# Optimization experiments

Measured on AMD Instinct MI355X. Metric: run time of the kernel, lower is better.

## Reference

```python
import jax, jax.numpy as jnp
import numpy as np


def dwconv1d(u, w, b):
    # u: (B, C, L), w: (C, 1, 3) depthwise, padding=1 -> same length
    out = jax.lax.conv_general_dilated(
        u, w, window_strides=(1,), padding=[(1, 1)],
        dimension_numbers=('NCH', 'OIH', 'NCH'),
        feature_group_count=u.shape[1])
    return out + b[None, :, None]


def selective_scan(u, delta, A, Bm, Cm, D, delta_bias):
    # u, delta: (B, KD, L); A: (KD, N); Bm, Cm: (B, K, N, L); D, delta_bias: (KD,)
    Bsz, KD, L = u.shape
    K, N = Bm.shape[1], Bm.shape[2]
    Dg = KD // K
    delta = jax.nn.softplus(delta + delta_bias[None, :, None])
    Bexp = jnp.repeat(Bm, Dg, axis=1)  # (B, KD, N, L)
    Cexp = jnp.repeat(Cm, Dg, axis=1)
    dA = jnp.exp(delta[:, :, None, :] * A[None, :, :, None])        # (B, KD, N, L)
    dBu = delta[:, :, None, :] * Bexp * u[:, :, None, :]            # (B, KD, N, L)

    def step(h, inp):
        a, bu, c = inp
        h = a * h + bu
        return h, jnp.sum(h * c, axis=-1)

    a_t = jnp.moveaxis(dA, -1, 0)
    bu_t = jnp.moveaxis(dBu, -1, 0)
    c_t = jnp.moveaxis(Cexp, -1, 0)
    _, ys = jax.lax.scan(step, jnp.zeros((Bsz, KD, N), u.dtype), (a_t, bu_t, c_t))
    return jnp.moveaxis(ys, 0, -1) + D[None, :, None] * u           # (B, KD, L)


def setup_inputs():
    key = jax.random.key(0)
    ks = jax.random.split(key, 8)
    d_inner, d_state, dt_rank, K = 192, 16, 6, 1
    bincounts = np.array([4096, 3000, 3500, 2500])
    total = int(bincounts.sum())
    max_bin = int(bincounts.max())
    starts = np.concatenate([[0], np.cumsum(bincounts)[:-1]])
    # compute_padding: wrap-around padded gather indices per cloud
    padded_idx = np.concatenate([np.arange(max_bin) % bc + st for bc, st in zip(bincounts, starts)])
    # crop-back indices into the (B*max_bin) padded layout
    valid_idx = np.concatenate([i * max_bin + np.arange(bc) for i, bc in enumerate(bincounts)])
    order = np.stack([np.random.RandomState(0).permutation(total)])
    inverse = np.argsort(order, axis=1)
    x = jax.random.normal(ks[0], (d_inner, total), jnp.float32)
    x_proj_weight = jax.random.normal(ks[1], (K, dt_rank + 2 * d_state, d_inner), jnp.float32) * 0.05
    dt_projs_weight = jax.random.normal(ks[2], (K, d_inner, dt_rank), jnp.float32) * 0.1
    dt_projs_bias = jax.random.normal(ks[3], (K, d_inner), jnp.float32) * 0.1
    A_logs = jnp.log(jnp.tile(jnp.arange(1, d_state + 1, dtype=jnp.float32), (K * d_inner, 1)))
    Ds = jnp.ones((K * d_inner,), jnp.float32)
    conv_w = jax.random.normal(ks[4], (K * d_inner, 1, 3), jnp.float32) * 0.2
    conv_b = jnp.zeros((K * d_inner,), jnp.float32)
    ln_gamma = jnp.ones((d_inner,), jnp.float32)
    ln_beta = jnp.zeros((d_inner,), jnp.float32)
    return {
        'x': x, 'x_proj_weight': x_proj_weight, 'dt_projs_weight': dt_projs_weight,
        'dt_projs_bias': dt_projs_bias, 'A_logs': A_logs, 'Ds': Ds,
        'conv_w': conv_w, 'conv_b': conv_b, 'ln_gamma': ln_gamma, 'ln_beta': ln_beta,
        'order': jnp.asarray(order, jnp.int32), 'inverse': jnp.asarray(inverse, jnp.int32),
        'padded_idx': jnp.asarray(padded_idx, jnp.int32),
        'valid_idx': jnp.asarray(valid_idx, jnp.int32), 'max_bin': max_bin,
    }


def reference(x, x_proj_weight, dt_projs_weight, dt_projs_bias, A_logs, Ds,
              conv_w, conv_b, ln_gamma, ln_beta,
              order, inverse, padded_idx, valid_idx, max_bin):
    K, Dch, R = dt_projs_weight.shape
    N = A_logs.shape[1]
    BM = padded_idx.shape[0]
    Bsz = BM // max_bin
    # multi-directional gather with offset padding: x[:, order[k]][:, padded_idx]
    idx = jnp.take(order, padded_idx, axis=1)                       # (K, B*max_bin)
    xs = jnp.take(x, idx, axis=1)                                   # (Dch, K, B*max_bin)
    xs = xs.transpose(1, 0, 2).reshape(K, Dch, Bsz, max_bin).transpose(2, 0, 1, 3)  # (B,K,D,L)
    x_dbl = jnp.einsum('bkdl,kcd->bkcl', xs, x_proj_weight)         # (B,K,R+2N,L)
    dts, Bs, Cs = jnp.split(x_dbl, [R, R + N], axis=2)
    dts = jnp.einsum('bkrl,kdr->bkdl', dts, dt_projs_weight)
    u = xs.reshape(Bsz, K * Dch, max_bin)
    delta = dts.reshape(Bsz, K * Dch, max_bin)
    A = -jnp.exp(A_logs)
    u = dwconv1d(u, conv_w, conv_b)  # conv1d applied after x_dbl/dts, before scan
    ys = selective_scan(u, delta, A, Bs, Cs, Ds, dt_projs_bias.reshape(-1))  # (B, K*Dch, L)
    # crop padding per cloud and concat along points
    ys = ys.reshape(Bsz, K, Dch, max_bin).transpose(1, 2, 0, 3).reshape(K, Dch, BM)
    ys = jnp.take(ys, valid_idx, axis=2)                            # (K, Dch, total)
    # K == 1, y_proj_weight is None -> scatter back through inverse permutation
    y = jnp.take(ys[0], inverse[0], axis=1)                         # (Dch, total)
    y = y.T                                                         # (total, Dch)
    mu = jnp.mean(y, axis=-1, keepdims=True)
    var = jnp.var(y, axis=-1, keepdims=True)
    y = (y - mu) / jnp.sqrt(var + 1e-5) * ln_gamma + ln_beta        # LayerNorm(d_inner)
    return y
```

## Files before the change

kernel.cpp:

```cpp
#include <hip/hip_runtime.h>
#include <math.h>

#define DINNER 192
#define NST    16
#define RNK    6
#define LSEQ   4096
#define BSZ    4
#define TOTAL  13096
#define BMPAD  16384
#define CL     32
#define MAXC   128
#define NSTATE 3072
#define NCHAIN 12288
#define NB32   410

#define BC_OF(b)  ((b)==0?4096:(b)==1?3000:(b)==2?3500:2500)
#define QST_OF(b) ((b)==0?0:(b)==1?4096:(b)==2?7096:10596)
#define NCB_OF(b) ((b)==0?128:(b)==1?94:(b)==2?110:79)

__device__ float  g_xs[(size_t)TOTAL * DINNER];
__device__ float  g_BC[(size_t)TOTAL * 32];
__device__ float  g_dt[(size_t)TOTAL * 8];
__device__ float2 g_PQ[(size_t)BSZ * MAXC * NSTATE];
__device__ float  g_hin[(size_t)BSZ * MAXC * NSTATE];

__global__ __launch_bounds__(256) void kA(
    const float* __restrict__ x, const float* __restrict__ W,
    const int* __restrict__ inverse)
{
    const int blk = blockIdx.x;
    const int t = threadIdx.x;
    const bool isG = (blk >= NB32);
    const int P0 = (isG ? blk - NB32 : blk) * 32;
    const int npts = min(32, TOTAL - P0);

    __shared__ float sx[32 * 193];
    __shared__ float sW[38 * DINNER];
    __shared__ int   sg[32];

    if (t < 32) sg[t] = (t < npts) ? inverse[P0 + t] : 0;

    float xt[24];
    #pragma unroll
    for (int k = 0; k < 24; ++k) {
        int idx = t + k * 256;
        int j = idx & 31, d = idx >> 5;
        xt[k] = (j < npts) ? x[(size_t)d * TOTAL + P0 + j] : 0.f;
    }
    float wt[29];
    if (isG) {
        #pragma unroll
        for (int k = 0; k < 29; ++k) {
            int idx = t + k * 256;
            wt[k] = (idx < 38 * DINNER) ? W[idx] : 0.f;
        }
    }
    #pragma unroll
    for (int k = 0; k < 24; ++k) {
        int idx = t + k * 256;
        int j = idx & 31, d = idx >> 5;
        sx[j * 193 + d] = xt[k];
    }
    if (isG) {
        #pragma unroll
        for (int k = 0; k < 29; ++k) {
            int idx = t + k * 256;
            if (idx < 38 * DINNER) sW[idx] = wt[k];
        }
    }
    __syncthreads();

    if (!isG) {
        for (int idx = t; idx < npts * 48; idx += 256) {
            int j = idx / 48, q = idx - j * 48;
            const float* sp = &sx[j * 193 + q * 4];
            float4 v = {sp[0], sp[1], sp[2], sp[3]};
            *(float4*)&g_xs[(size_t)sg[j] * DINNER + q * 4] = v;
        }
    } else {
        const int j = t & 31, cw = t >> 5;
        float acc[5] = {0.f, 0.f, 0.f, 0.f, 0.f};
        for (int dt0 = 0; dt0 < DINNER; dt0 += 16) {
            float xr[16];
            #pragma unroll
            for (int q = 0; q < 16; ++q) xr[q] = sx[j * 193 + dt0 + q];
            #pragma unroll
            for (int k = 0; k < 5; ++k) {
                const int c = cw + 8 * k;
                if (c < RNK + 2 * NST) {
                    const float4* wr = (const float4*)&sW[c * DINNER + dt0];
                    float4 w0 = wr[0], w1 = wr[1], w2 = wr[2], w3 = wr[3];
                    float a = acc[k];
                    a += xr[0]*w0.x + xr[1]*w0.y + xr[2]*w0.z + xr[3]*w0.w;
                    a += xr[4]*w1.x + xr[5]*w1.y + xr[6]*w1.z + xr[7]*w1.w;
                    a += xr[8]*w2.x + xr[9]*w2.y + xr[10]*w2.z + xr[11]*w2.w;
                    a += xr[12]*w3.x + xr[13]*w3.y + xr[14]*w3.z + xr[15]*w3.w;
                    acc[k] = a;
                }
            }
        }
        if (j < npts) {
            const int g = sg[j];
            #pragma unroll
            for (int k = 0; k < 5; ++k) {
                const int c = cw + 8 * k;
                if (c < RNK)                g_dt[(size_t)g * 8 + c] = acc[k];
                else if (c < RNK + 2 * NST) g_BC[(size_t)g * 32 + (c - RNK)] = acc[k];
            }
        }
    }
}

__global__ __launch_bounds__(192) void k2_scan1(
    const float* __restrict__ A_logs, const float* __restrict__ conv_w,
    const float* __restrict__ conv_b, const float* __restrict__ dtW,
    const float* __restrict__ dtB)
{
    const int blk = blockIdx.x;
    const int b = blk >> 7;
    const int chunk = blk & (MAXC - 1);
    const int bc = BC_OF(b), qst = QST_OF(b), ncb = NCB_OF(b);
    if (chunk >= ncb) return;
    const int l0 = chunk * CL;
    const int steps = min(CL, bc - l0);
    const int t = threadIdx.x;

    __shared__ float sxr[(CL + 2) * DINNER];
    __shared__ float sB[CL * NST];
    __shared__ float sdt[CL * 8];

    float xr[CL + 2];
    #pragma unroll
    for (int k = 0; k < CL + 2; ++k) {
        int pos = l0 - 1 + k;
        bool v = (k < steps + 2) && (pos >= 0) && (pos < LSEQ);
        int pw = (pos >= bc) ? pos - bc : pos;
        xr[k] = v ? g_xs[(size_t)(qst + pw) * DINNER + t] : 0.f;
    }
    float bv[3];
    #pragma unroll
    for (int k = 0; k < 3; ++k) {
        int idx = t + k * 192;
        bv[k] = (idx < steps * NST)
              ? g_BC[(size_t)(qst + l0 + (idx >> 4)) * 32 + (idx & 15)] : 0.f;
    }
    float dv[2];
    #pragma unroll
    for (int k = 0; k < 2; ++k) {
        int idx = t + k * 192;
        dv[k] = (idx < steps * 8) ? g_dt[(size_t)(qst + l0) * 8 + idx] : 0.f;
    }
    #pragma unroll
    for (int k = 0; k < CL + 2; ++k) sxr[k * DINNER + t] = xr[k];
    #pragma unroll
    for (int k = 0; k < 3; ++k) {
        int idx = t + k * 192;
        if (idx < CL * NST) sB[idx] = bv[k];
    }
    #pragma unroll
    for (int k = 0; k < 2; ++k) {
        int idx = t + k * 192;
        if (idx < CL * 8) sdt[idx] = dv[k];
    }
    __syncthreads();

    float Av[16];
    {
        const float4* A4 = (const float4*)(A_logs + t * NST);
        #pragma unroll
        for (int q = 0; q < 4; ++q) {
            float4 v = A4[q];
            Av[q*4+0] = -__expf(v.x); Av[q*4+1] = -__expf(v.y);
            Av[q*4+2] = -__expf(v.z); Av[q*4+3] = -__expf(v.w);
        }
    }
    const float Av0 = Av[0];
    bool fast = true;
    #pragma unroll
    for (int n = 0; n < 16; ++n)
        fast = fast && (fabsf(Av[n] - (float)(n + 1) * Av0) <= 1e-4f * (float)(n + 1));

    float wdt[RNK];
    #pragma unroll
    for (int r = 0; r < RNK; ++r) wdt[r] = dtW[t * RNK + r];
    const float bdel = dtB[t];
    const float cw0 = conv_w[t*3+0], cw1 = conv_w[t*3+1], cw2 = conv_w[t*3+2];
    const float cb = conv_b[t];

    float h[16];
    #pragma unroll
    for (int n = 0; n < 16; ++n) h[n] = 0.f;
    float delsum = 0.f;
    float xm = sxr[t], xc = sxr[DINNER + t];

    for (int i = 0; i < steps; ++i) {
        float xp = sxr[(i + 2) * DINNER + t];
        float u = fmaf(cw0, xm, fmaf(cw1, xc, fmaf(cw2, xp, cb)));
        float da = bdel;
        #pragma unroll
        for (int r = 0; r < RNK; ++r) da = fmaf(wdt[r], sdt[i * 8 + r], da);
        float del = (da > 20.f) ? da : log1pf(__expf(da));
        float du = del * u;
        delsum += del;
        const float4* b4 = (const float4*)&sB[i * NST];
        float4 B0 = b4[0], B1 = b4[1], B2 = b4[2], B3 = b4[3];
        const float Bv[16] = {B0.x,B0.y,B0.z,B0.w, B1.x,B1.y,B1.z,B1.w,
                              B2.x,B2.y,B2.z,B2.w, B3.x,B3.y,B3.z,B3.w};
        if (fast) {
            float e = __expf(del * Av0);
            float a = e;
            #pragma unroll
            for (int n = 0; n < 16; ++n) { h[n] = fmaf(a, h[n], Bv[n] * du); a *= e; }
        } else {
            #pragma unroll
            for (int n = 0; n < 16; ++n) {
                float a = __expf(del * Av[n]);
                h[n] = fmaf(a, h[n], Bv[n] * du);
            }
        }
        xm = xc; xc = xp;
    }

    float4* o4 = (float4*)(g_PQ + (size_t)(b * MAXC + chunk) * NSTATE + t * 16);
    #pragma unroll
    for (int k = 0; k < 8; ++k) {
        float P0v = __expf(Av[2*k]   * delsum);
        float P1v = __expf(Av[2*k+1] * delsum);
        o4[k] = make_float4(P0v, h[2*k], P1v, h[2*k+1]);
    }
}

__global__ __launch_bounds__(128) void k3_comb()
{
    const int gid = blockIdx.x * 128 + threadIdx.x;
    const int b = gid / NSTATE;
    const int s = gid - b * NSTATE;
    const int ncb = NCB_OF(b);
    float h = 0.f;
    for (int c0 = 0; c0 < MAXC; c0 += 16) {
        if (c0 >= ncb) break;
        float2 v[16];
        #pragma unroll
        for (int k = 0; k < 16; ++k) {
            int c = c0 + k;
            v[k] = (c < ncb) ? g_PQ[(size_t)(b * MAXC + c) * NSTATE + s]
                             : make_float2(1.f, 0.f);
        }
        #pragma unroll
        for (int k = 0; k < 16; ++k) {
            int c = c0 + k;
            if (c < ncb) g_hin[(size_t)(b * MAXC + c) * NSTATE + s] = h;
            h = fmaf(v[k].x, h, v[k].y);
        }
    }
}

__global__ __launch_bounds__(192) void k4_scan2(
    const float* __restrict__ A_logs, const float* __restrict__ conv_w,
    const float* __restrict__ conv_b, const float* __restrict__ dtW,
    const float* __restrict__ dtB, const float* __restrict__ Ds,
    const int* __restrict__ order, const float* __restrict__ gamma,
    const float* __restrict__ beta, float* __restrict__ out)
{
    const int blk = blockIdx.x;
    const int b = blk >> 7;
    const int chunk = blk & (MAXC - 1);
    const int bc = BC_OF(b), qst = QST_OF(b), ncb = NCB_OF(b);
    if (chunk >= ncb) return;
    const int l0 = chunk * CL;
    const int steps = min(CL, bc - l0);
    const int t = threadIdx.x;

    __shared__ float sxr[(CL + 2) * DINNER];
    __shared__ float sBC[CL * 32];
    __shared__ float sdt[CL * 8];
    __shared__ float sy[CL * DINNER];

    float xr[CL + 2];
    #pragma unroll
    for (int k = 0; k < CL + 2; ++k) {
        int pos = l0 - 1 + k;
        bool v = (k < steps + 2) && (pos >= 0) && (pos < LSEQ);
        int pw = (pos >= bc) ? pos - bc : pos;
        xr[k] = v ? g_xs[(size_t)(qst + pw) * DINNER + t] : 0.f;
    }
    float bcv[6];
    #pragma unroll
    for (int k = 0; k < 6; ++k) {
        int idx = t + k * 192;
        bcv[k] = (idx < steps * 32) ? g_BC[(size_t)(qst + l0) * 32 + idx] : 0.f;
    }
    float dv[2];
    #pragma unroll
    for (int k = 0; k < 2; ++k) {
        int idx = t + k * 192;
        dv[k] = (idx < steps * 8) ? g_dt[(size_t)(qst + l0) * 8 + idx] : 0.f;
    }
    float h[16];
    {
        const float4* h4 = (const float4*)(g_hin + (size_t)(b * MAXC + chunk) * NSTATE + t * 16);
        #pragma unroll
        for (int q = 0; q < 4; ++q) *(float4*)&h[q * 4] = h4[q];
    }
    #pragma unroll
    for (int k = 0; k < CL + 2; ++k) sxr[k * DINNER + t] = xr[k];
    #pragma unroll
    for (int k = 0; k < 6; ++k) {
        int idx = t + k * 192;
        if (idx < CL * 32) sBC[idx] = bcv[k];
    }
    #pragma unroll
    for (int k = 0; k < 2; ++k) {
        int idx = t + k * 192;
        if (idx < CL * 8) sdt[idx] = dv[k];
    }
    __syncthreads();

    float Av[16];
    {
        const float4* A4 = (const float4*)(A_logs + t * NST);
        #pragma unroll
        for (int q = 0; q < 4; ++q) {
            float4 v = A4[q];
            Av[q*4+0] = -__expf(v.x); Av[q*4+1] = -__expf(v.y);
            Av[q*4+2] = -__expf(v.z); Av[q*4+3] = -__expf(v.w);
        }
    }
    const float Av0 = Av[0];
    bool fast = true;
    #pragma unroll
    for (int n = 0; n < 16; ++n)
        fast = fast && (fabsf(Av[n] - (float)(n + 1) * Av0) <= 1e-4f * (float)(n + 1));

    float wdt[RNK];
    #pragma unroll
    for (int r = 0; r < RNK; ++r) wdt[r] = dtW[t * RNK + r];
    const float bdel = dtB[t];
    const float cw0 = conv_w[t*3+0], cw1 = conv_w[t*3+1], cw2 = conv_w[t*3+2];
    const float cb = conv_b[t];
    const float Dd = Ds[t];

    float xm = sxr[t], xc = sxr[DINNER + t];

    for (int i = 0; i < steps; ++i) {
        float xp = sxr[(i + 2) * DINNER + t];
        float u = fmaf(cw0, xm, fmaf(cw1, xc, fmaf(cw2, xp, cb)));
        float da = bdel;
        #pragma unroll
        for (int r = 0; r < RNK; ++r) da = fmaf(wdt[r], sdt[i * 8 + r], da);
        float del = (da > 20.f) ? da : log1pf(__expf(da));
        float du = del * u;
        const float4* b4 = (const float4*)&sBC[i * 32];
        float4 B0 = b4[0], B1 = b4[1], B2 = b4[2], B3 = b4[3];
        float4 C0 = b4[4], C1 = b4[5], C2 = b4[6], C3 = b4[7];
        const float Bv[16] = {B0.x,B0.y,B0.z,B0.w, B1.x,B1.y,B1.z,B1.w,
                              B2.x,B2.y,B2.z,B2.w, B3.x,B3.y,B3.z,B3.w};
        const float Cv[16] = {C0.x,C0.y,C0.z,C0.w, C1.x,C1.y,C1.z,C1.w,
                              C2.x,C2.y,C2.z,C2.w, C3.x,C3.y,C3.z,C3.w};
        float y = Dd * u;
        if (fast) {
            float e = __expf(del * Av0);
            float a = e;
            #pragma unroll
            for (int n = 0; n < 16; ++n) {
                h[n] = fmaf(a, h[n], Bv[n] * du);
                y = fmaf(h[n], Cv[n], y);
                a *= e;
            }
        } else {
            #pragma unroll
            for (int n = 0; n < 16; ++n) {
                float a = __expf(del * Av[n]);
                h[n] = fmaf(a, h[n], Bv[n] * du);
                y = fmaf(h[n], Cv[n], y);
            }
        }
        sy[i * DINNER + t] = y;
        xm = xc; xc = xp;
    }
    __syncthreads();

    const int wv = t >> 6;
    const int lane = t & 63;
    for (int i = wv; i < steps; i += 3) {
        const float v0 = sy[i * DINNER + lane];
        const float v1 = sy[i * DINNER + 64 + lane];
        const float v2 = sy[i * DINNER + 128 + lane];
        float s  = v0 + v1 + v2;
        float s2 = v0 * v0 + v1 * v1 + v2 * v2;
        #pragma unroll
        for (int off = 1; off < 64; off <<= 1) {
            s  += __shfl_xor(s,  off);
            s2 += __shfl_xor(s2, off);
        }
        const float mu   = s / (float)DINNER;
        const float var  = s2 / (float)DINNER - mu * mu;
        const float rstd = rsqrtf(var + 1e-5f);
        const int p = order[qst + l0 + i];
        float* orow = out + (size_t)p * DINNER;
        orow[lane]       = (v0 - mu) * rstd * gamma[lane]       + beta[lane];
        orow[lane + 64]  = (v1 - mu) * rstd * gamma[lane + 64]  + beta[lane + 64];
        orow[lane + 128] = (v2 - mu) * rstd * gamma[lane + 128] + beta[lane + 128];
    }
}

extern "C" void kernel_launch(void* const* d_in, const int* in_sizes, int n_in,
                              void* d_out, int out_size, void* d_ws, size_t ws_size,
                              hipStream_t stream) {
    const float* x       = (const float*)d_in[0];
    const float* W       = (const float*)d_in[1];
    const float* dtW     = (const float*)d_in[2];
    const float* dtB     = (const float*)d_in[3];
    const float* A_logs  = (const float*)d_in[4];
    const float* Ds      = (const float*)d_in[5];
    const float* conv_w  = (const float*)d_in[6];
    const float* conv_b  = (const float*)d_in[7];
    const float* gamma   = (const float*)d_in[8];
    const float* beta    = (const float*)d_in[9];
    const int*   order   = (const int*)d_in[10];
    const int*   inverse = (const int*)d_in[11];
    float* outp = (float*)d_out;

    if (in_sizes[0] != TOTAL * DINNER || in_sizes[12] != BMPAD) return;

    kA<<<2 * NB32, 256, 0, stream>>>(x, W, inverse);
    k2_scan1<<<BSZ * MAXC, 192, 0, stream>>>(A_logs, conv_w, conv_b, dtW, dtB);
    k3_comb<<<NCHAIN / 128, 128, 0, stream>>>();
    k4_scan2<<<BSZ * MAXC, 192, 0, stream>>>(A_logs, conv_w, conv_b, dtW, dtB,
                                             Ds, order, gamma, beta, outp);
}
```

Baseline: 178.7 us.

## Merge kA gather/projection blocks, keep x window in registers, use power tree

```diff
diff --git a/kernel.cpp b/kernel.cpp
--- a/kernel.cpp
+++ b/kernel.cpp
@@ -24,15 +24,21 @@
 __device__ float2 g_PQ[(size_t)BSZ * MAXC * NSTATE];
 __device__ float  g_hin[(size_t)BSZ * MAXC * NSTATE];
 
+#define POWER_TREE(e, a)                                                   \
+    { float e1 = (e);                                                      \
+      float e2 = e1*e1, e4 = e2*e2, e8 = e4*e4;                            \
+      a[0]=e1;      a[1]=e2;      a[2]=e2*e1;   a[3]=e4;                   \
+      a[4]=e4*e1;   a[5]=e4*e2;   a[6]=e4*a[2]; a[7]=e8;                   \
+      a[8]=e8*e1;   a[9]=e8*e2;   a[10]=e8*a[2];a[11]=e8*e4;               \
+      a[12]=e8*a[4];a[13]=e8*a[5];a[14]=e8*a[6];a[15]=e8*e8; }
+
 __global__ __launch_bounds__(256) void kA(
     const float* __restrict__ x, const float* __restrict__ W,
     const int* __restrict__ inverse)
 {
-    const int blk = blockIdx.x;
+    const int P0 = blockIdx.x * 32;
+    const int npts = min(32, TOTAL - P0);
     const int t = threadIdx.x;
-    const bool isG = (blk >= NB32);
-    const int P0 = (isG ? blk - NB32 : blk) * 32;
-    const int npts = min(32, TOTAL - P0);
 
     __shared__ float sx[32 * 193];
     __shared__ float sW[38 * DINNER];
@@ -48,65 +54,58 @@
         xt[k] = (j < npts) ? x[(size_t)d * TOTAL + P0 + j] : 0.f;
     }
     float wt[29];
-    if (isG) {
-        #pragma unroll
-        for (int k = 0; k < 29; ++k) {
-            int idx = t + k * 256;
-            wt[k] = (idx < 38 * DINNER) ? W[idx] : 0.f;
-        }
+    #pragma unroll
+    for (int k = 0; k < 29; ++k) {
+        int idx = t + k * 256;
+        wt[k] = (idx < 38 * DINNER) ? W[idx] : 0.f;
     }
     #pragma unroll
     for (int k = 0; k < 24; ++k) {
         int idx = t + k * 256;
-        int j = idx & 31, d = idx >> 5;
-        sx[j * 193 + d] = xt[k];
-    }
-    if (isG) {
-        #pragma unroll
-        for (int k = 0; k < 29; ++k) {
-            int idx = t + k * 256;
-            if (idx < 38 * DINNER) sW[idx] = wt[k];
-        }
+        sx[(idx & 31) * 193 + (idx >> 5)] = xt[k];
+    }
+    #pragma unroll
+    for (int k = 0; k < 29; ++k) {
+        int idx = t + k * 256;
+        if (idx < 38 * DINNER) sW[idx] = wt[k];
     }
     __syncthreads();
 
-    if (!isG) {
-        for (int idx = t; idx < npts * 48; idx += 256) {
-            int j = idx / 48, q = idx - j * 48;
-            const float* sp = &sx[j * 193 + q * 4];
-            float4 v = {sp[0], sp[1], sp[2], sp[3]};
-            *(float4*)&g_xs[(size_t)sg[j] * DINNER + q * 4] = v;
-        }
-    } else {
-        const int j = t & 31, cw = t >> 5;
-        float acc[5] = {0.f, 0.f, 0.f, 0.f, 0.f};
-        for (int dt0 = 0; dt0 < DINNER; dt0 += 16) {
-            float xr[16];
-            #pragma unroll
-            for (int q = 0; q < 16; ++q) xr[q] = sx[j * 193 + dt0 + q];
-            #pragma unroll
-            for (int k = 0; k < 5; ++k) {
-                const int c = cw + 8 * k;
-                if (c < RNK + 2 * NST) {
-                    const float4* wr = (const float4*)&sW[c * DINNER + dt0];
-                    float4 w0 = wr[0], w1 = wr[1], w2 = wr[2], w3 = wr[3];
-                    float a = acc[k];
-                    a += xr[0]*w0.x + xr[1]*w0.y + xr[2]*w0.z + xr[3]*w0.w;
-                    a += xr[4]*w1.x + xr[5]*w1.y + xr[6]*w1.z + xr[7]*w1.w;
-                    a += xr[8]*w2.x + xr[9]*w2.y + xr[10]*w2.z + xr[11]*w2.w;
-                    a += xr[12]*w3.x + xr[13]*w3.y + xr[14]*w3.z + xr[15]*w3.w;
-                    acc[k] = a;
-                }
+    for (int idx = t; idx < npts * 48; idx += 256) {
+        int j = idx / 48, q = idx - j * 48;
+        const float* sp = &sx[j * 193 + q * 4];
+        float4 v = {sp[0], sp[1], sp[2], sp[3]};
+        *(float4*)&g_xs[(size_t)sg[j] * DINNER + q * 4] = v;
+    }
+
+    const int j = t & 31, cw = t >> 5;
+    float acc[5] = {0.f, 0.f, 0.f, 0.f, 0.f};
+    for (int dt0 = 0; dt0 < DINNER; dt0 += 16) {
+        float xr[16];
+        #pragma unroll
+        for (int q = 0; q < 16; ++q) xr[q] = sx[j * 193 + dt0 + q];
+        #pragma unroll
+        for (int k = 0; k < 5; ++k) {
+            const int c = cw + 8 * k;
+            if (c < RNK + 2 * NST) {
+                const float4* wr = (const float4*)&sW[c * DINNER + dt0];
+                float4 w0 = wr[0], w1 = wr[1], w2 = wr[2], w3 = wr[3];
+                float a = acc[k];
+                a += xr[0]*w0.x + xr[1]*w0.y + xr[2]*w0.z + xr[3]*w0.w;
+                a += xr[4]*w1.x + xr[5]*w1.y + xr[6]*w1.z + xr[7]*w1.w;
+                a += xr[8]*w2.x + xr[9]*w2.y + xr[10]*w2.z + xr[11]*w2.w;
+                a += xr[12]*w3.x + xr[13]*w3.y + xr[14]*w3.z + xr[15]*w3.w;
+                acc[k] = a;
             }
         }
-        if (j < npts) {
-            const int g = sg[j];
-            #pragma unroll
-            for (int k = 0; k < 5; ++k) {
-                const int c = cw + 8 * k;
-                if (c < RNK)                g_dt[(size_t)g * 8 + c] = acc[k];
-                else if (c < RNK + 2 * NST) g_BC[(size_t)g * 32 + (c - RNK)] = acc[k];
-            }
+    }
+    if (j < npts) {
+        const int g = sg[j];
+        #pragma unroll
+        for (int k = 0; k < 5; ++k) {
+            const int c = cw + 8 * k;
+            if (c < RNK)                g_dt[(size_t)g * 8 + c] = acc[k];
+            else if (c < RNK + 2 * NST) g_BC[(size_t)g * 32 + (c - RNK)] = acc[k];
         }
     }
 }
@@ -125,7 +124,6 @@
     const int steps = min(CL, bc - l0);
     const int t = threadIdx.x;
 
-    __shared__ float sxr[(CL + 2) * DINNER];
     __shared__ float sB[CL * NST];
     __shared__ float sdt[CL * 8];
 
@@ -151,8 +149,6 @@
         dv[k] = (idx < steps * 8) ? g_dt[(size_t)(qst + l0) * 8 + idx] : 0.f;
     }
     #pragma unroll
-    for (int k = 0; k < CL + 2; ++k) sxr[k * DINNER + t] = xr[k];
-    #pragma unroll
     for (int k = 0; k < 3; ++k) {
         int idx = t + k * 192;
         if (idx < CL * NST) sB[idx] = bv[k];
@@ -191,15 +187,15 @@
     #pragma unroll
     for (int n = 0; n < 16; ++n) h[n] = 0.f;
     float delsum = 0.f;
-    float xm = sxr[t], xc = sxr[DINNER + t];
-
-    for (int i = 0; i < steps; ++i) {
-        float xp = sxr[(i + 2) * DINNER + t];
-        float u = fmaf(cw0, xm, fmaf(cw1, xc, fmaf(cw2, xp, cb)));
+
+    #pragma unroll
+    for (int i = 0; i < CL; ++i) {
+        float u = fmaf(cw0, xr[i], fmaf(cw1, xr[i + 1], fmaf(cw2, xr[i + 2], cb)));
         float da = bdel;
         #pragma unroll
         for (int r = 0; r < RNK; ++r) da = fmaf(wdt[r], sdt[i * 8 + r], da);
         float del = (da > 20.f) ? da : log1pf(__expf(da));
+        if (i >= steps) del = 0.f;
         float du = del * u;
         delsum += del;
         const float4* b4 = (const float4*)&sB[i * NST];
@@ -207,10 +203,10 @@
         const float Bv[16] = {B0.x,B0.y,B0.z,B0.w, B1.x,B1.y,B1.z,B1.w,
                               B2.x,B2.y,B2.z,B2.w, B3.x,B3.y,B3.z,B3.w};
         if (fast) {
-            float e = __expf(del * Av0);
-            float a = e;
+            float a[16];
+            POWER_TREE(__expf(del * Av0), a);
             #pragma unroll
-            for (int n = 0; n < 16; ++n) { h[n] = fmaf(a, h[n], Bv[n] * du); a *= e; }
+            for (int n = 0; n < 16; ++n) h[n] = fmaf(a[n], h[n], Bv[n] * du);
         } else {
             #pragma unroll
             for (int n = 0; n < 16; ++n) {
@@ -218,7 +214,6 @@
                 h[n] = fmaf(a, h[n], Bv[n] * du);
             }
         }
-        xm = xc; xc = xp;
     }
 
     float4* o4 = (float4*)(g_PQ + (size_t)(b * MAXC + chunk) * NSTATE + t * 16);
@@ -271,10 +266,9 @@
     const int steps = min(CL, bc - l0);
     const int t = threadIdx.x;
 
-    __shared__ float sxr[(CL + 2) * DINNER];
+    __shared__ float sy[CL * DINNER];
     __shared__ float sBC[CL * 32];
     __shared__ float sdt[CL * 8];
-    __shared__ float sy[CL * DINNER];
 
     float xr[CL + 2];
     #pragma unroll
@@ -303,8 +297,6 @@
         for (int q = 0; q < 4; ++q) *(float4*)&h[q * 4] = h4[q];
     }
     #pragma unroll
-    for (int k = 0; k < CL + 2; ++k) sxr[k * DINNER + t] = xr[k];
-    #pragma unroll
     for (int k = 0; k < 6; ++k) {
         int idx = t + k * 192;
         if (idx < CL * 32) sBC[idx] = bcv[k];
@@ -340,15 +332,14 @@
     const float cb = conv_b[t];
     const float Dd = Ds[t];
 
-    float xm = sxr[t], xc = sxr[DINNER + t];
-
-    for (int i = 0; i < steps; ++i) {
-        float xp = sxr[(i + 2) * DINNER + t];
-        float u = fmaf(cw0, xm, fmaf(cw1, xc, fmaf(cw2, xp, cb)));
+    #pragma unroll
+    for (int i = 0; i < CL; ++i) {
+        float u = fmaf(cw0, xr[i], fmaf(cw1, xr[i + 1], fmaf(cw2, xr[i + 2], cb)));
         float da = bdel;
         #pragma unroll
         for (int r = 0; r < RNK; ++r) da = fmaf(wdt[r], sdt[i * 8 + r], da);
         float del = (da > 20.f) ? da : log1pf(__expf(da));
+        if (i >= steps) del = 0.f;
         float du = del * u;
         const float4* b4 = (const float4*)&sBC[i * 32];
         float4 B0 = b4[0], B1 = b4[1], B2 = b4[2], B3 = b4[3];
@@ -359,13 +350,12 @@
                               C2.x,C2.y,C2.z,C2.w, C3.x,C3.y,C3.z,C3.w};
         float y = Dd * u;
         if (fast) {
-            float e = __expf(del * Av0);
-            float a = e;
+            float a[16];
+            POWER_TREE(__expf(del * Av0), a);
             #pragma unroll
             for (int n = 0; n < 16; ++n) {
-                h[n] = fmaf(a, h[n], Bv[n] * du);
+                h[n] = fmaf(a[n], h[n], Bv[n] * du);
                 y = fmaf(h[n], Cv[n], y);
-                a *= e;
             }
         } else {
             #pragma unroll
@@ -376,7 +366,6 @@
             }
         }
         sy[i * DINNER + t] = y;
-        xm = xc; xc = xp;
     }
     __syncthreads();
 
@@ -423,7 +412,7 @@
 
     if (in_sizes[0] != TOTAL * DINNER || in_sizes[12] != BMPAD) return;
 
-    kA<<<2 * NB32, 256, 0, stream>>>(x, W, inverse);
+    kA<<<NB32, 256, 0, stream>>>(x, W, inverse);
     k2_scan1<<<BSZ * MAXC, 192, 0, stream>>>(A_logs, conv_w, conv_b, dtW, dtB);
     k3_comb<<<NCHAIN / 128, 128, 0, stream>>>();
     k4_scan2<<<BSZ * MAXC, 192, 0, stream>>>(A_logs, conv_w, conv_b, dtW, dtB,
```

Result: no change. 175.7 us (-1.7%).
